# Kernel optimization log

Hardware: AMD Instinct MI355X
Metric: run time of the kernel (lower is better)

The kernel has to match this reference:

```python
import jax, jax.numpy as jnp
import numpy as np

B, T, H, OUT = 2048, 256, 512, 1


def setup_inputs() -> dict:
    key = jax.random.key(0)
    ks = jax.random.split(key, 11)
    s = 1.0 / np.sqrt(H)
    return {
        "x": jax.random.normal(ks[0], (B, T), dtype=jnp.float32),
        # weights stored as (in, out), i.e. torch Linear weight transposed
        "Wx0": jax.random.normal(ks[1], (1, H), dtype=jnp.float32) * s,
        "bx0": jax.random.normal(ks[2], (H,), dtype=jnp.float32) * s,
        "Wh0": jax.random.normal(ks[3], (H, H), dtype=jnp.float32) * s,
        "bh0": jax.random.normal(ks[4], (H,), dtype=jnp.float32) * s,
        "Wx1": jax.random.normal(ks[5], (H, H), dtype=jnp.float32) * s,
        "bx1": jax.random.normal(ks[6], (H,), dtype=jnp.float32) * s,
        "Wh1": jax.random.normal(ks[7], (H, H), dtype=jnp.float32) * s,
        "bh1": jax.random.normal(ks[8], (H,), dtype=jnp.float32) * s,
        "Wfc": jax.random.normal(ks[9], (H, OUT), dtype=jnp.float32) * s,
        "bfc": jax.random.normal(ks[10], (OUT,), dtype=jnp.float32) * s,
    }


def reference(x, Wx0, bx0, Wh0, bh0, Wx1, bx1, Wh1, bh1, Wfc, bfc):
    # Stacked 2-layer Elman RNN: h_l[t] = tanh(W_in_l @ in + b_in_l + W_h_l @ h_l[t-1] + b_h_l)
    batch = x.shape[0]
    hdim = Wh0.shape[0]
    h0 = jnp.zeros((batch, hdim), dtype=x.dtype)
    h1 = jnp.zeros((batch, hdim), dtype=x.dtype)

    def step(carry, xt):
        h0, h1 = carry
        # layer 0: scalar input per timestep -> outer product with Wx0 row
        h0 = jnp.tanh(xt[:, None] * Wx0[0] + bx0 + h0 @ Wh0 + bh0)
        # layer 1 consumes the NEW h0 (matches the in-place loop in torch)
        h1 = jnp.tanh(h0 @ Wx1 + bx1 + h1 @ Wh1 + bh1)
        return (h0, h1), None

    (h0, h1), _ = jax.lax.scan(step, (h0, h1), x.T)  # scan over time [T, B]
    return h1 @ Wfc + bfc  # [B, OUT]
```

## Files before the change

kernel.cpp:

```cpp
#include <hip/hip_runtime.h>
#include <hip/hip_bf16.h>


typedef _Float16 half8 __attribute__((ext_vector_type(8)));
typedef float f32x4 __attribute__((ext_vector_type(4)));

#define T_STEPS 256
#define H_DIM   512
#define BM      16

#define AS1 __attribute__((address_space(1)))
#define AS3 __attribute__((address_space(3)))

#define VMW8 asm volatile("s_waitcnt vmcnt(8)" ::: "memory")
#define VMW0 asm volatile("s_waitcnt vmcnt(0)" ::: "memory")
#define BARRIER() do { \
    asm volatile("s_waitcnt lgkmcnt(0)" ::: "memory"); \
    __builtin_amdgcn_s_barrier(); \
    asm volatile("" ::: "memory"); \
  } while (0)

__device__ __forceinline__ float tanh_fast(float z){
  float az = fabsf(z);
  float e  = __expf(-2.0f * az);
  float r  = (1.0f - e) * __builtin_amdgcn_rcpf(1.0f + e);
  return copysignf(r, z);
}

__global__ void prep_w_45028437131357(const float* __restrict__ W,
                                      half8* __restrict__ out){
  int tid  = blockIdx.x * 256 + threadIdx.x;
  int lane = tid & 63;
  int kc   = (tid >> 6) & 15;
  int nt   = tid >> 10;
  int col  = nt * 16 + (lane & 15);
  int k0   = kc * 32 + (lane >> 4) * 8;
  half8 v;
#pragma unroll
  for (int j = 0; j < 8; ++j) v[j] = (_Float16)W[(k0 + j) * H_DIM + col];
  out[tid] = v;
}

__device__ __forceinline__ void stage_g(int g, int koff, const half8* W0,
                                        const half8* W1, const half8* WX,
                                        char* Sw, int w4, int lane){
  int g48 = (g >= 48) ? g - 48 : g;
  const half8* M = (g48 < 16) ? W0 : ((g48 < 32) ? W1 : WX);
  int keff = ((g48 & 15) + koff) & 15;
  char* dst = Sw + (g % 3) * 4096;
#pragma unroll
  for (int i = 0; i < 4; ++i)
    __builtin_amdgcn_global_load_lds(
        (const AS1 void*)(M + ((w4 + i) * 16 + keff) * 64 + lane),
        (AS3 void*)(dst + i * 1024), 16, 0, 0);
}


__global__ __launch_bounds__(512, 2)
void rnn_main_45028437131357(const float* __restrict__ x,
                             const float* __restrict__ Wx0,
                             const float* __restrict__ bx0,
                             const float* __restrict__ bh0,
                             const float* __restrict__ bx1,
                             const float* __restrict__ bh1,
                             const float* __restrict__ Wfc,
                             const float* __restrict__ bfc,
                             const half8* __restrict__ Wh0f,
                             const half8* __restrict__ Wx1f,
                             const half8* __restrict__ Wh1f,
                             float* __restrict__ out){
  __shared__ __align__(16) char  h0s[BM * 1024];
  __shared__ __align__(16) char  h1s[BM * 1024];
  __shared__ __align__(16) float xall[BM * 256];
  __shared__ __align__(16) char  Ss[8 * 3 * 4096];

  const int tid  = threadIdx.x;
  const int lane = tid & 63;
  const int w    = tid >> 6;
  const int w4   = 4 * w;
  const int r0   = blockIdx.x * BM;
  const int koff = (blockIdx.x >> 3) & 15;
  char* Sw = Ss + w * 12288;

  for (int i = tid; i < BM * 256; i += 512){
    ((float*)h0s)[i] = 0.0f;
    ((float*)h1s)[i] = 0.0f;
    int r = i >> 8, c = i & 255;
    xall[r * 256 + (c ^ ((r & 7) << 2))] = x[(r0 + r) * T_STEPS + c];
  }

  const int cl      = lane & 15;
  const int kg      = lane >> 4;
  const int aBase   = cl * 1024 + kg * 16;
  const int aSwz    = (cl & 7) << 4;
  const int rowBase = kg * 4;

  float wx0c[4], b0c[4], b1c[4];
  int   colA[4];
#pragma unroll
  for (int i = 0; i < 4; ++i){
    int col = (w4 + i) * 16 + cl;
    colA[i] = col;
    wx0c[i] = Wx0[col];
    b0c[i]  = bx0[col] + bh0[col];
    b1c[i]  = bx1[col] + bh1[col];
  }

  stage_g(0, koff, Wh0f, Wh1f, Wx1f, Sw, w4, lane);
  stage_g(1, koff, Wh0f, Wh1f, Wx1f, Sw, w4, lane);

  const f32x4 z4 = {0.f, 0.f, 0.f, 0.f};

#define CONSUME(APTR, ACC, KC, G)                                             \
    {                                                                         \
      int keff = ((KC) + koff) & 15;                                          \
      const char* sb = Sw + ((G) % 3) * 4096;                                 \
      half8 a   = *(const half8*)((APTR) + ((aBase + keff * 64) ^ aSwz));     \
      half8 bb0 = *(const half8*)(sb +    0 + lane * 16);                     \
      half8 bb1 = *(const half8*)(sb + 1024 + lane * 16);                     \
      half8 bb2 = *(const half8*)(sb + 2048 + lane * 16);                     \
      half8 bb3 = *(const half8*)(sb + 3072 + lane * 16);                     \
      ACC[0] = __builtin_amdgcn_mfma_f32_16x16x32_f16(a, bb0, ACC[0], 0,0,0); \
      ACC[1] = __builtin_amdgcn_mfma_f32_16x16x32_f16(a, bb1, ACC[1], 0,0,0); \
      ACC[2] = __builtin_amdgcn_mfma_f32_16x16x32_f16(a, bb2, ACC[2], 0,0,0); \
      ACC[3] = __builtin_amdgcn_mfma_f32_16x16x32_f16(a, bb3, ACC[3], 0,0,0); \
    }

  for (int t = 0; t < T_STEPS; ++t){
    BARRIER();

    f32x4 acc0[4] = {z4, z4, z4, z4};
    f32x4 acc1[4] = {z4, z4, z4, z4};

#pragma unroll
    for (int kc = 0; kc < 16; ++kc){
      stage_g(kc + 2, koff, Wh0f, Wh1f, Wx1f, Sw, w4, lane);
      VMW8;
      CONSUME(h0s, acc0, kc, kc);
    }
#pragma unroll
    for (int kc = 0; kc < 16; ++kc){
      stage_g(18 + kc, koff, Wh0f, Wh1f, Wx1f, Sw, w4, lane);
      VMW8;
      CONSUME(h1s, acc1, kc, 16 + kc);
    }

    _Float16 nh0[4][4];
    {
      float xv[4];
#pragma unroll
      for (int rg = 0; rg < 4; ++rg){
        int row = rowBase + rg;
        xv[rg] = xall[row * 256 + (t ^ ((row & 7) << 2))];
      }
#pragma unroll
      for (int i = 0; i < 4; ++i)
#pragma unroll
        for (int rg = 0; rg < 4; ++rg)
          nh0[i][rg] = (_Float16)tanh_fast(acc0[i][rg] + b0c[i] + xv[rg] * wx0c[i]);
    }
    BARRIER();
#pragma unroll
    for (int i = 0; i < 4; ++i)
#pragma unroll
      for (int rg = 0; rg < 4; ++rg){
        int row = rowBase + rg;
        *(_Float16*)(h0s + row * 1024 +
                     ((colA[i] * 2) ^ ((row & 7) << 4))) = nh0[i][rg];
      }
    BARRIER();

#pragma unroll
    for (int kc = 0; kc < 16; ++kc){
      stage_g(34 + kc, koff, Wh0f, Wh1f, Wx1f, Sw, w4, lane);
      VMW8;
      CONSUME(h0s, acc1, kc, 32 + kc);
    }

#pragma unroll
    for (int i = 0; i < 4; ++i)
#pragma unroll
      for (int rg = 0; rg < 4; ++rg){
        int row = rowBase + rg;
        *(_Float16*)(h1s + row * 1024 +
                     ((colA[i] * 2) ^ ((row & 7) << 4))) =
            (_Float16)tanh_fast(acc1[i][rg] + b1c[i]);
      }
  }
#undef CONSUME
  VMW0;
  BARRIER();

  {
    int r  = tid >> 5;
    int g2 = tid & 31;
    float p = 0.0f;
#pragma unroll
    for (int k2 = 0; k2 < 16; ++k2){
      int c = g2 + 32 * k2;
      float hv = (float)*(const _Float16*)(h1s + r * 1024 +
                                           ((c * 2) ^ ((r & 7) << 4)));
      p += hv * Wfc[c];
    }
#pragma unroll
    for (int off = 16; off >= 1; off >>= 1) p += __shfl_xor(p, off);
    if (g2 == 0) out[r0 + r] = p + bfc[0];
  }
}

extern "C" void kernel_launch(void* const* d_in, const int* in_sizes, int n_in,
                              void* d_out, int out_size, void* d_ws, size_t ws_size,
                              hipStream_t stream) {
  const float* x   = (const float*)d_in[0];
  const float* Wx0 = (const float*)d_in[1];
  const float* bx0 = (const float*)d_in[2];
  const float* Wh0 = (const float*)d_in[3];
  const float* bh0 = (const float*)d_in[4];
  const float* Wx1 = (const float*)d_in[5];
  const float* bx1 = (const float*)d_in[6];
  const float* Wh1 = (const float*)d_in[7];
  const float* bh1 = (const float*)d_in[8];
  const float* Wfc = (const float*)d_in[9];
  const float* bfc = (const float*)d_in[10];

  _Float16* wsH = (_Float16*)d_ws;
  half8* Wh0f = (half8*)(wsH);
  half8* Wx1f = (half8*)(wsH + 262144);
  half8* Wh1f = (half8*)(wsH + 524288);

  prep_w_45028437131357<<<128, 256, 0, stream>>>(Wh0, Wh0f);
  prep_w_45028437131357<<<128, 256, 0, stream>>>(Wx1, Wx1f);
  prep_w_45028437131357<<<128, 256, 0, stream>>>(Wh1, Wh1f);

  rnn_main_45028437131357<<<128, 512, 0, stream>>>(
      x, Wx0, bx0, bh0, bx1, bh1, Wfc, bfc,
      (const half8*)Wh0f, (const half8*)Wx1f, (const half8*)Wh1f,
      (float*)d_out);
}
```

Measured before the change: 12.32 ms.

## Stream weights into registers instead of LDS and double-buffer layer-0 hidden state

Replaces the global-to-LDS weight staging with direct global_load_dwordx4 into a 4-deep register ring, with vmcnt waits and sched barriers ahead of the MFMAs. The layer-0 hidden state is double-buffered, which removes one barrier per timestep and lets tanh results be written straight to LDS. An LDS padding array is added, likely to hold occupancy at one block per CU or to change the LDS footprint. The change raises register pressure, and the raw asm loads with hand-written waitcnt rely on the compiler not reordering them.

```diff
diff --git a/kernel.cpp b/kernel.cpp
--- a/kernel.cpp
+++ b/kernel.cpp
@@ -9,16 +9,17 @@
 #define H_DIM   512
 #define BM      16
 
-#define AS1 __attribute__((address_space(1)))
-#define AS3 __attribute__((address_space(3)))
-
-#define VMW8 asm volatile("s_waitcnt vmcnt(8)" ::: "memory")
-#define VMW0 asm volatile("s_waitcnt vmcnt(0)" ::: "memory")
 #define BARRIER() do { \
     asm volatile("s_waitcnt lgkmcnt(0)" ::: "memory"); \
     __builtin_amdgcn_s_barrier(); \
     asm volatile("" ::: "memory"); \
   } while (0)
+
+__device__ __forceinline__ half8 gld16(const half8* p){
+  half8 r;
+  asm volatile("global_load_dwordx4 %0, %1, off" : "=v"(r) : "v"(p));
+  return r;
+}
 
 __device__ __forceinline__ float tanh_fast(float z){
   float az = fabsf(z);
@@ -39,20 +40,6 @@
 #pragma unroll
   for (int j = 0; j < 8; ++j) v[j] = (_Float16)W[(k0 + j) * H_DIM + col];
   out[tid] = v;
-}
-
-__device__ __forceinline__ void stage_g(int g, int koff, const half8* W0,
-                                        const half8* W1, const half8* WX,
-                                        char* Sw, int w4, int lane){
-  int g48 = (g >= 48) ? g - 48 : g;
-  const half8* M = (g48 < 16) ? W0 : ((g48 < 32) ? W1 : WX);
-  int keff = ((g48 & 15) + koff) & 15;
-  char* dst = Sw + (g % 3) * 4096;
-#pragma unroll
-  for (int i = 0; i < 4; ++i)
-    __builtin_amdgcn_global_load_lds(
-        (const AS1 void*)(M + ((w4 + i) * 16 + keff) * 64 + lane),
-        (AS3 void*)(dst + i * 1024), 16, 0, 0);
 }
 
 
@@ -69,10 +56,10 @@
                              const half8* __restrict__ Wx1f,
                              const half8* __restrict__ Wh1f,
                              float* __restrict__ out){
-  __shared__ __align__(16) char  h0s[BM * 1024];
+  __shared__ __align__(16) char  h0d[2][BM * 1024];
   __shared__ __align__(16) char  h1s[BM * 1024];
   __shared__ __align__(16) float xall[BM * 256];
-  __shared__ __align__(16) char  Ss[8 * 3 * 4096];
+  __shared__ char lds_pad[20 * 1024];
 
   const int tid  = threadIdx.x;
   const int lane = tid & 63;
@@ -80,10 +67,11 @@
   const int w4   = 4 * w;
   const int r0   = blockIdx.x * BM;
   const int koff = (blockIdx.x >> 3) & 15;
-  char* Sw = Ss + w * 12288;
+
+  if (out == nullptr) ((volatile char*)lds_pad)[0] = 1;
 
   for (int i = tid; i < BM * 256; i += 512){
-    ((float*)h0s)[i] = 0.0f;
+    ((float*)h0d[0])[i] = 0.0f;
     ((float*)h1s)[i] = 0.0f;
     int r = i >> 8, c = i & 255;
     xall[r * 256 + (c ^ ((r & 7) << 2))] = x[(r0 + r) * T_STEPS + c];
@@ -106,46 +94,58 @@
     b1c[i]  = bx1[col] + bh1[col];
   }
 
-  stage_g(0, koff, Wh0f, Wh1f, Wx1f, Sw, w4, lane);
-  stage_g(1, koff, Wh0f, Wh1f, Wx1f, Sw, w4, lane);
+  half8 rb[4][4];
+
+#define STAGE(G)                                                              \
+  {                                                                           \
+    int g48 = ((G) >= 48) ? (G) - 48 : (G);                                   \
+    const half8* M = (g48 < 16) ? Wh0f : ((g48 < 32) ? Wh1f : Wx1f);          \
+    int keff = ((g48 & 15) + koff) & 15;                                      \
+    const half8* base = M + keff * 64 + lane;                                 \
+    rb[(G) & 3][0] = gld16(base + (w4 + 0) * 1024);                           \
+    rb[(G) & 3][1] = gld16(base + (w4 + 1) * 1024);                           \
+    rb[(G) & 3][2] = gld16(base + (w4 + 2) * 1024);                           \
+    rb[(G) & 3][3] = gld16(base + (w4 + 3) * 1024);                           \
+  }
+
+#define CONSUME(APTR, ACC, KC, G)                                             \
+  {                                                                           \
+    int keff = (((KC) + koff) & 15);                                          \
+    half8 a = *(const half8*)((APTR) + ((aBase + keff * 64) ^ aSwz));         \
+    asm volatile("s_waitcnt vmcnt(12)");                                      \
+    __builtin_amdgcn_sched_barrier(0);                                        \
+    ACC[0] = __builtin_amdgcn_mfma_f32_16x16x32_f16(a, rb[(G)&3][0], ACC[0], 0,0,0); \
+    ACC[1] = __builtin_amdgcn_mfma_f32_16x16x32_f16(a, rb[(G)&3][1], ACC[1], 0,0,0); \
+    ACC[2] = __builtin_amdgcn_mfma_f32_16x16x32_f16(a, rb[(G)&3][2], ACC[2], 0,0,0); \
+    ACC[3] = __builtin_amdgcn_mfma_f32_16x16x32_f16(a, rb[(G)&3][3], ACC[3], 0,0,0); \
+  }
+
+  asm volatile("s_waitcnt vmcnt(0)" ::: "memory");
+  STAGE(0); STAGE(1); STAGE(2);
 
   const f32x4 z4 = {0.f, 0.f, 0.f, 0.f};
-
-#define CONSUME(APTR, ACC, KC, G)                                             \
-    {                                                                         \
-      int keff = ((KC) + koff) & 15;                                          \
-      const char* sb = Sw + ((G) % 3) * 4096;                                 \
-      half8 a   = *(const half8*)((APTR) + ((aBase + keff * 64) ^ aSwz));     \
-      half8 bb0 = *(const half8*)(sb +    0 + lane * 16);                     \
-      half8 bb1 = *(const half8*)(sb + 1024 + lane * 16);                     \
-      half8 bb2 = *(const half8*)(sb + 2048 + lane * 16);                     \
-      half8 bb3 = *(const half8*)(sb + 3072 + lane * 16);                     \
-      ACC[0] = __builtin_amdgcn_mfma_f32_16x16x32_f16(a, bb0, ACC[0], 0,0,0); \
-      ACC[1] = __builtin_amdgcn_mfma_f32_16x16x32_f16(a, bb1, ACC[1], 0,0,0); \
-      ACC[2] = __builtin_amdgcn_mfma_f32_16x16x32_f16(a, bb2, ACC[2], 0,0,0); \
-      ACC[3] = __builtin_amdgcn_mfma_f32_16x16x32_f16(a, bb3, ACC[3], 0,0,0); \
-    }
+  int s = 0;
 
   for (int t = 0; t < T_STEPS; ++t){
     BARRIER();
 
+    const char* h0cur = h0d[s];
+    char*       h0nxt = h0d[s ^ 1];
+
     f32x4 acc0[4] = {z4, z4, z4, z4};
     f32x4 acc1[4] = {z4, z4, z4, z4};
 
 #pragma unroll
     for (int kc = 0; kc < 16; ++kc){
-      stage_g(kc + 2, koff, Wh0f, Wh1f, Wx1f, Sw, w4, lane);
-      VMW8;
-      CONSUME(h0s, acc0, kc, kc);
+      STAGE(kc + 3);
+      CONSUME(h0cur, acc0, kc, kc);
     }
 #pragma unroll
     for (int kc = 0; kc < 16; ++kc){
-      stage_g(18 + kc, koff, Wh0f, Wh1f, Wx1f, Sw, w4, lane);
-      VMW8;
-      CONSUME(h1s, acc1, kc, 16 + kc);
-    }
-
-    _Float16 nh0[4][4];
+      STAGE(kc + 19);
+      CONSUME(h1s, acc1, kc, kc + 16);
+    }
+
     {
       float xv[4];
 #pragma unroll
@@ -156,25 +156,19 @@
 #pragma unroll
       for (int i = 0; i < 4; ++i)
 #pragma unroll
-        for (int rg = 0; rg < 4; ++rg)
-          nh0[i][rg] = (_Float16)tanh_fast(acc0[i][rg] + b0c[i] + xv[rg] * wx0c[i]);
+        for (int rg = 0; rg < 4; ++rg){
+          float z = acc0[i][rg] + b0c[i] + xv[rg] * wx0c[i];
+          int row = rowBase + rg;
+          *(_Float16*)(h0nxt + row * 1024 +
+                       ((colA[i] * 2) ^ ((row & 7) << 4))) = (_Float16)tanh_fast(z);
+        }
     }
     BARRIER();
-#pragma unroll
-    for (int i = 0; i < 4; ++i)
-#pragma unroll
-      for (int rg = 0; rg < 4; ++rg){
-        int row = rowBase + rg;
-        *(_Float16*)(h0s + row * 1024 +
-                     ((colA[i] * 2) ^ ((row & 7) << 4))) = nh0[i][rg];
-      }
-    BARRIER();
 
 #pragma unroll
     for (int kc = 0; kc < 16; ++kc){
-      stage_g(34 + kc, koff, Wh0f, Wh1f, Wx1f, Sw, w4, lane);
-      VMW8;
-      CONSUME(h0s, acc1, kc, 32 + kc);
+      STAGE(kc + 35);
+      CONSUME(h0nxt, acc1, kc, kc + 32);
     }
 
 #pragma unroll
@@ -186,9 +180,12 @@
                      ((colA[i] * 2) ^ ((row & 7) << 4))) =
             (_Float16)tanh_fast(acc1[i][rg] + b1c[i]);
       }
-  }
+    s ^= 1;
+  }
+#undef STAGE
 #undef CONSUME
-  VMW0;
+
+  asm volatile("s_waitcnt vmcnt(0)" ::: "memory");
   BARRIER();
 
   {
```

After: 13.07 ms. 6.0% more time.
